# Optimization experiments

Measured on AMD Instinct MI355X. Metric: run time of the kernel, lower is better.

## Reference

```python
import jax, jax.numpy as jnp
import numpy as np

T = 2048          # total tokens
H = 2560          # hidden_size
E = 8             # experts per modality
TOPK = 2          # moe_k
I_TXT = 1536      # moe_intermediate_size[0]
I_IMG = 512       # moe_intermediate_size[1]
I_SH = I_TXT * 2  # shared experts intermediate (moe_num_shared_experts=2)


def setup_inputs() -> dict:
    key = jax.random.key(0)
    ks = jax.random.split(key, 12)
    s = 0.02
    return {
        "hidden_states": jax.random.normal(ks[0], (T, H), jnp.float32),
        "visual_token_mask": jax.random.randint(ks[1], (T, 1), 0, 2).astype(bool),
        # text modality: router gate [E,H], SwiGLU experts [E,H,I]/[E,I,H]
        "text_gate_w": jax.random.normal(ks[2], (E, H), jnp.float32) * s,
        "text_wg": jax.random.normal(ks[3], (E, H, I_TXT), jnp.float32) * s,
        "text_wu": jax.random.normal(ks[4], (E, H, I_TXT), jnp.float32) * s,
        "text_wd": jax.random.normal(ks[5], (E, I_TXT, H), jnp.float32) * s,
        # image modality
        "image_gate_w": jax.random.normal(ks[6], (E, H), jnp.float32) * s,
        "image_wg": jax.random.normal(ks[7], (E, H, I_IMG), jnp.float32) * s,
        "image_wu": jax.random.normal(ks[8], (E, H, I_IMG), jnp.float32) * s,
        "image_wd": jax.random.normal(ks[9], (E, I_IMG, H), jnp.float32) * s,
        # shared experts MLP (dense SwiGLU)
        "sh_wg": jax.random.normal(ks[10], (H, I_SH), jnp.float32) * s,
        "sh_wu": jax.random.normal(ks[11], (H, I_SH), jnp.float32) * s,
        "sh_wd": jax.random.normal(jax.random.fold_in(key, 99), (I_SH, H), jnp.float32) * s,
    }


def _moe(x, gate_w, wg, wu, wd):
    """FusedMoE: softmax router -> top-k -> renormalize -> SwiGLU experts -> combine.
    x: [T,H]; gate_w: [E,H]; wg/wu: [E,H,I]; wd: [E,I,H]."""
    logits = jnp.einsum("th,eh->te", x, gate_w)                 # [T,E]
    probs = jax.nn.softmax(logits.astype(jnp.float32), axis=-1)
    topv, topi = jax.lax.top_k(probs, TOPK)                      # [T,K]
    topv = topv / jnp.sum(topv, axis=-1, keepdims=True)          # renormalize=True
    # dense per-token expert weights [T,E] (zero for unselected experts)
    w = jnp.sum(jax.nn.one_hot(topi, probs.shape[-1], dtype=topv.dtype)
                * topv[..., None], axis=1)
    g = jnp.einsum("th,ehi->tei", x, wg)                         # [T,E,I]
    u = jnp.einsum("th,ehi->tei", x, wu)
    h = jax.nn.silu(g) * u
    y = jnp.einsum("tei,eih->teh", h, wd)                        # [T,E,H]
    return jnp.einsum("te,teh->th", w.astype(x.dtype), y)


def _shared_mlp(x, wg, wu, wd):
    return (jax.nn.silu(x @ wg) * (x @ wu)) @ wd


def reference(hidden_states, visual_token_mask,
              text_gate_w, text_wg, text_wu, text_wd,
              image_gate_w, image_wg, image_wu, image_wd,
              sh_wg, sh_wu, sh_wd):
    x = hidden_states.reshape(-1, hidden_states.shape[-1])       # [T,H]
    shared_out = _shared_mlp(x, sh_wg, sh_wu, sh_wd)
    text_out = _moe(x, text_gate_w, text_wg, text_wu, text_wd)
    image_out = _moe(x, image_gate_w, image_wg, image_wu, image_wd)
    vmask = visual_token_mask.reshape(-1, 1)                     # [T,1] bool
    # scatter-combine: image experts on visual tokens, text experts elsewhere
    final = jnp.where(vmask, image_out, text_out) + shared_out
    return final.reshape(hidden_states.shape)
```

## Files before the change

### kernel.cpp

```cpp
#include <hip/hip_runtime.h>
#include <hip/hip_bf16.h>

#define T 2048
#define H 2560
#define NE 8
#define ITXT 1536
#define IIMG 512
#define ISH 3072
#define CAP 2048

using bf16 = __hip_bfloat16;
typedef short short8 __attribute__((ext_vector_type(8)));
typedef float float4v __attribute__((ext_vector_type(4)));

static constexpr size_t OFF_XBF  = 0;
static constexpr size_t OFF_CNT  = OFF_XBF + (size_t)T * H * 2;
static constexpr size_t OFF_TOK  = OFF_CNT + 128;
static constexpr size_t OFF_WTS  = OFF_TOK + (size_t)17 * CAP * 4;
static constexpr size_t OFF_HTXT = OFF_WTS + (size_t)17 * CAP * 4;
static constexpr size_t OFF_HIMG = OFF_HTXT + (size_t)NE * CAP * ITXT * 2;
static constexpr size_t OFF_HSH  = OFF_HIMG + (size_t)NE * CAP * IIMG * 2;

__device__ __forceinline__ unsigned short f2bf(float f) {
    bf16 b = __float2bfloat16(f);
    unsigned short u;
    __builtin_memcpy(&u, &b, 2);
    return u;
}

__global__ void k_cast_init(const float* __restrict__ x, bf16* __restrict__ xb,
                            int* __restrict__ counts, int* __restrict__ toks,
                            float* __restrict__ wts) {
    int i = blockIdx.x * blockDim.x + threadIdx.x;
    float4 v = ((const float4*)x)[i];
    ushort4 p;
    p.x = f2bf(v.x); p.y = f2bf(v.y); p.z = f2bf(v.z); p.w = f2bf(v.w);
    *(ushort4*)(xb + 4 * (size_t)i) = p;
    if (i < CAP) { toks[16 * CAP + i] = i; wts[16 * CAP + i] = 1.0f; }
    if (i == 0) counts[16] = T;
}

__global__ void k_router(const float* __restrict__ x, const int* __restrict__ vmask,
                         const float* __restrict__ tg, const float* __restrict__ ig,
                         int* __restrict__ counts, int* __restrict__ toks,
                         float* __restrict__ wts) {
    int wave = threadIdx.x >> 6;
    int lane = threadIdx.x & 63;
    int t = blockIdx.x * 4 + wave;
    if (t >= T) return;
    bool vis = vmask[t] != 0;
    const float* gw = vis ? ig : tg;
    const float* xr = x + (size_t)t * H;
    float logits[NE];
#pragma unroll
    for (int e = 0; e < NE; ++e) {
        const float* g = gw + (size_t)e * H;
        double s = 0.0;
        for (int h = lane; h < H; h += 64) s += (double)xr[h] * (double)g[h];
#pragma unroll
        for (int off = 32; off > 0; off >>= 1) s += __shfl_xor(s, off);
        logits[e] = (float)s;
    }
    if (lane == 0) {
        int e1 = 0;
#pragma unroll
        for (int e = 1; e < NE; ++e) if (logits[e] > logits[e1]) e1 = e;
        int e2 = -1;
#pragma unroll
        for (int e = 0; e < NE; ++e)
            if (e != e1 && (e2 < 0 || logits[e] > logits[e2])) e2 = e;
        float w1 = 1.0f / (1.0f + expf(logits[e2] - logits[e1]));
        float w2 = 1.0f - w1;
        int b = vis ? 8 : 0;
        int s1 = atomicAdd(&counts[b + e1], 1);
        toks[(b + e1) * CAP + s1] = t; wts[(b + e1) * CAP + s1] = w1;
        int s2 = atomicAdd(&counts[b + e2], 1);
        toks[(b + e2) * CAP + s2] = t; wts[(b + e2) * CAP + s2] = w2;
    }
}

#define MT 128
#define NT 64
#define BK 32
#define LSTR 40

__global__ __launch_bounds__(256) void k_gateup_all(
    const float* __restrict__ twg, const float* __restrict__ twu,
    const float* __restrict__ iwg, const float* __restrict__ iwu,
    const float* __restrict__ swg, const float* __restrict__ swu,
    const bf16* __restrict__ A,
    const int* __restrict__ counts, const int* __restrict__ toks,
    bf16* __restrict__ htxt, bf16* __restrict__ himg, bf16* __restrict__ hsh) {
    int z = blockIdx.z;
    const float *bg, *bu; int N; bf16* hb;
    if (z < 8) {
        bg = twg + (size_t)z * H * ITXT; bu = twu + (size_t)z * H * ITXT;
        N = ITXT; hb = htxt + (size_t)z * CAP * ITXT;
    } else if (z < 16) {
        int e = z - 8;
        bg = iwg + (size_t)e * H * IIMG; bu = iwu + (size_t)e * H * IIMG;
        N = IIMG; hb = himg + (size_t)e * CAP * IIMG;
    } else {
        bg = swg; bu = swu; N = ISH; hb = hsh;
    }
    int n0 = blockIdx.x * NT;
    if (n0 >= N) return;
    int cnt = counts[z];
    int m0 = blockIdx.y * MT;
    if (m0 >= cnt) return;
    const int* tk = toks + (size_t)z * CAP + m0;

    __shared__ bf16 As[2][MT][LSTR];
    __shared__ bf16 Bs[2][2][NT][LSTR];

    int tid = threadIdx.x;
    int lane = tid & 63;
    int wv = tid >> 6;
    int wm = wv >> 1, wn = wv & 1;

    int ar = tid >> 2;
    int akc = (tid & 3) << 3;
    int bn = (tid & 15) << 2;
    int bk = (tid >> 4) << 1;
    int fr = lane & 15;
    int fk = (lane >> 4) << 3;

    int cl = cnt - m0 - 1;
    int r0 = ar, r1 = ar + 64;
    int t0 = tk[r0 < cl ? r0 : cl];
    int t1 = tk[r1 < cl ? r1 : cl];
    const bf16* aP0 = A + (size_t)t0 * H + akc;
    const bf16* aP1 = A + (size_t)t1 * H + akc;
    const float* pg = bg + (size_t)bk * N + n0 + bn;
    const float* pu = bu + (size_t)bk * N + n0 + bn;

    float4v accg[4][2], accu[4][2];
#pragma unroll
    for (int i = 0; i < 4; ++i)
#pragma unroll
        for (int j = 0; j < 2; ++j) { accg[i][j] = (float4v)0.0f; accu[i][j] = (float4v)0.0f; }

    uint4 a0r, a1r; float4 g0r, g1r, u0r, u1r;
    auto LOADR = [&](int k0) {
        a0r = *(const uint4*)(aP0 + k0);
        a1r = *(const uint4*)(aP1 + k0);
        const float* g = pg + (size_t)k0 * N;
        g0r = *(const float4*)g; g1r = *(const float4*)(g + N);
        const float* u = pu + (size_t)k0 * N;
        u0r = *(const float4*)u; u1r = *(const float4*)(u + N);
    };
    auto STORER = [&](int buf) {
        *(uint4*)&As[buf][ar][akc] = a0r;
        *(uint4*)&As[buf][ar + 64][akc] = a1r;
        *(unsigned*)&Bs[buf][0][bn + 0][bk] = (unsigned)f2bf(g0r.x) | ((unsigned)f2bf(g1r.x) << 16);
        *(unsigned*)&Bs[buf][0][bn + 1][bk] = (unsigned)f2bf(g0r.y) | ((unsigned)f2bf(g1r.y) << 16);
        *(unsigned*)&Bs[buf][0][bn + 2][bk] = (unsigned)f2bf(g0r.z) | ((unsigned)f2bf(g1r.z) << 16);
        *(unsigned*)&Bs[buf][0][bn + 3][bk] = (unsigned)f2bf(g0r.w) | ((unsigned)f2bf(g1r.w) << 16);
        *(unsigned*)&Bs[buf][1][bn + 0][bk] = (unsigned)f2bf(u0r.x) | ((unsigned)f2bf(u1r.x) << 16);
        *(unsigned*)&Bs[buf][1][bn + 1][bk] = (unsigned)f2bf(u0r.y) | ((unsigned)f2bf(u1r.y) << 16);
        *(unsigned*)&Bs[buf][1][bn + 2][bk] = (unsigned)f2bf(u0r.z) | ((unsigned)f2bf(u1r.z) << 16);
        *(unsigned*)&Bs[buf][1][bn + 3][bk] = (unsigned)f2bf(u0r.w) | ((unsigned)f2bf(u1r.w) << 16);
    };

    LOADR(0);
    STORER(0);
    int cur = 0;
    for (int k0 = 0; k0 < H; k0 += BK) {
        __syncthreads();
        bool more = (k0 + BK) < H;
        if (more) LOADR(k0 + BK);
        short8 af[4], bgf[2], buf_[2];
#pragma unroll
        for (int i = 0; i < 4; ++i) af[i] = *(const short8*)&As[cur][wm * 64 + i * 16 + fr][fk];
#pragma unroll
        for (int j = 0; j < 2; ++j) {
            bgf[j]  = *(const short8*)&Bs[cur][0][wn * 32 + j * 16 + fr][fk];
            buf_[j] = *(const short8*)&Bs[cur][1][wn * 32 + j * 16 + fr][fk];
        }
#pragma unroll
        for (int i = 0; i < 4; ++i)
#pragma unroll
            for (int j = 0; j < 2; ++j) {
                accg[i][j] = __builtin_amdgcn_mfma_f32_16x16x32_bf16(af[i], bgf[j],  accg[i][j], 0, 0, 0);
                accu[i][j] = __builtin_amdgcn_mfma_f32_16x16x32_bf16(af[i], buf_[j], accu[i][j], 0, 0, 0);
            }
        if (more) STORER(cur ^ 1);
        cur ^= 1;
    }

    int rbase = (lane >> 4) << 2;
    int cc = lane & 15;
#pragma unroll
    for (int i = 0; i < 4; ++i)
#pragma unroll
        for (int j = 0; j < 2; ++j)
#pragma unroll
            for (int r = 0; r < 4; ++r) {
                int ml = m0 + wm * 64 + i * 16 + rbase + r;
                if (ml < cnt) {
                    int col = n0 + wn * 32 + j * 16 + cc;
                    float g = accg[i][j][r], u = accu[i][j][r];
                    float hv = g / (1.0f + expf(-g)) * u;
                    hb[(size_t)ml * N + col] = __float2bfloat16(hv);
                }
            }
}

__global__ __launch_bounds__(256) void k_down_all(
    const float* __restrict__ twd, const float* __restrict__ iwd, const float* __restrict__ swd,
    const bf16* __restrict__ htxt, const bf16* __restrict__ himg, const bf16* __restrict__ hsh,
    const int* __restrict__ counts, const int* __restrict__ toks,
    const float* __restrict__ wts,
    float* __restrict__ out) {
    int z = blockIdx.z;
    const float* bw; const bf16* Ab; int K;
    if (z < 8) {
        bw = twd + (size_t)z * ITXT * H; Ab = htxt + (size_t)z * CAP * ITXT; K = ITXT;
    } else if (z < 16) {
        int e = z - 8;
        bw = iwd + (size_t)e * IIMG * H; Ab = himg + (size_t)e * CAP * IIMG; K = IIMG;
    } else {
        bw = swd; Ab = hsh; K = ISH;
    }
    int cnt = counts[z];
    int m0 = blockIdx.y * MT;
    if (m0 >= cnt) return;
    int n0 = blockIdx.x * NT;

    __shared__ bf16 As[2][MT][LSTR];
    __shared__ bf16 Bs[2][NT][LSTR];

    int tid = threadIdx.x;
    int lane = tid & 63;
    int wv = tid >> 6;
    int wm = wv >> 1, wn = wv & 1;

    int ar = tid >> 2;
    int akc = (tid & 3) << 3;
    int bn = (tid & 15) << 2;
    int bk = (tid >> 4) << 1;
    int fr = lane & 15;
    int fk = (lane >> 4) << 3;

    const bf16* aP0 = Ab + (size_t)(m0 + ar) * K + akc;
    const bf16* aP1 = Ab + (size_t)(m0 + ar + 64) * K + akc;
    const float* pb = bw + (size_t)bk * H + n0 + bn;

    float4v acc[4][2];
#pragma unroll
    for (int i = 0; i < 4; ++i)
#pragma unroll
        for (int j = 0; j < 2; ++j) acc[i][j] = (float4v)0.0f;

    uint4 a0r, a1r; float4 b0r, b1r;
    auto LOADR = [&](int k0) {
        a0r = *(const uint4*)(aP0 + k0);
        a1r = *(const uint4*)(aP1 + k0);
        const float* s = pb + (size_t)k0 * H;
        b0r = *(const float4*)s; b1r = *(const float4*)(s + H);
    };
    auto STORER = [&](int buf) {
        *(uint4*)&As[buf][ar][akc] = a0r;
        *(uint4*)&As[buf][ar + 64][akc] = a1r;
        *(unsigned*)&Bs[buf][bn + 0][bk] = (unsigned)f2bf(b0r.x) | ((unsigned)f2bf(b1r.x) << 16);
        *(unsigned*)&Bs[buf][bn + 1][bk] = (unsigned)f2bf(b0r.y) | ((unsigned)f2bf(b1r.y) << 16);
        *(unsigned*)&Bs[buf][bn + 2][bk] = (unsigned)f2bf(b0r.z) | ((unsigned)f2bf(b1r.z) << 16);
        *(unsigned*)&Bs[buf][bn + 3][bk] = (unsigned)f2bf(b0r.w) | ((unsigned)f2bf(b1r.w) << 16);
    };

    LOADR(0);
    STORER(0);
    int cur = 0;
    for (int k0 = 0; k0 < K; k0 += BK) {
        __syncthreads();
        bool more = (k0 + BK) < K;
        if (more) LOADR(k0 + BK);
        short8 af[4], bf_[2];
#pragma unroll
        for (int i = 0; i < 4; ++i) af[i] = *(const short8*)&As[cur][wm * 64 + i * 16 + fr][fk];
#pragma unroll
        for (int j = 0; j < 2; ++j) bf_[j] = *(const short8*)&Bs[cur][wn * 32 + j * 16 + fr][fk];
#pragma unroll
        for (int i = 0; i < 4; ++i)
#pragma unroll
            for (int j = 0; j < 2; ++j)
                acc[i][j] = __builtin_amdgcn_mfma_f32_16x16x32_bf16(af[i], bf_[j], acc[i][j], 0, 0, 0);
        if (more) STORER(cur ^ 1);
        cur ^= 1;
    }

    int rbase = (lane >> 4) << 2;
    int cc = lane & 15;
    const int* tkl = toks + (size_t)z * CAP;
    const float* wl = wts + (size_t)z * CAP;
#pragma unroll
    for (int i = 0; i < 4; ++i)
#pragma unroll
        for (int j = 0; j < 2; ++j)
#pragma unroll
            for (int r = 0; r < 4; ++r) {
                int ml = m0 + wm * 64 + i * 16 + rbase + r;
                if (ml < cnt) {
                    int col = n0 + wn * 32 + j * 16 + cc;
                    int tok = tkl[ml];
                    atomicAdd(&out[(size_t)tok * H + col], acc[i][j][r] * wl[ml]);
                }
            }
}

extern "C" void kernel_launch(void* const* d_in, const int* in_sizes, int n_in,
                              void* d_out, int out_size, void* d_ws, size_t ws_size,
                              hipStream_t stream) {
    const float* x    = (const float*)d_in[0];
    const int*   vm   = (const int*)d_in[1];
    const float* tg   = (const float*)d_in[2];
    const float* twg  = (const float*)d_in[3];
    const float* twu  = (const float*)d_in[4];
    const float* twd  = (const float*)d_in[5];
    const float* ig   = (const float*)d_in[6];
    const float* iwg  = (const float*)d_in[7];
    const float* iwu  = (const float*)d_in[8];
    const float* iwd  = (const float*)d_in[9];
    const float* swg  = (const float*)d_in[10];
    const float* swu  = (const float*)d_in[11];
    const float* swd  = (const float*)d_in[12];
    float* out = (float*)d_out;
    char* ws = (char*)d_ws;

    bf16* xb     = (bf16*)(ws + OFF_XBF);
    int*  counts = (int*)(ws + OFF_CNT);
    int*  toks   = (int*)(ws + OFF_TOK);
    float* wtsp  = (float*)(ws + OFF_WTS);
    bf16* htxt   = (bf16*)(ws + OFF_HTXT);
    bf16* himg   = (bf16*)(ws + OFF_HIMG);
    bf16* hsh    = (bf16*)(ws + OFF_HSH);

    hipMemsetAsync(counts, 0, 128, stream);
    hipMemsetAsync(out, 0, (size_t)T * H * sizeof(float), stream);

    k_cast_init<<<dim3((T * H / 4) / 256), dim3(256), 0, stream>>>(x, xb, counts, toks, wtsp);
    k_router<<<dim3(T / 4), dim3(256), 0, stream>>>(x, vm, tg, ig, counts, toks, wtsp);

    k_gateup_all<<<dim3(ISH / NT, CAP / MT, 17), dim3(256), 0, stream>>>(
        twg, twu, iwg, iwu, swg, swu, xb, counts, toks, htxt, himg, hsh);

    k_down_all<<<dim3(H / NT, CAP / MT, 17), dim3(256), 0, stream>>>(
        twd, iwd, swd, htxt, himg, hsh, counts, toks, wtsp, out);
}
```

Measured before the change: 1.134 ms.

## Pre-transpose weights to bf16 K-major with swizzled LDS and BK=64

Adds a per-call transpose kernel that converts every fp32 weight matrix into bf16 laid out N-major with K contiguous. The GEMMs then load weights with 16-byte vector loads and skip the in-loop fp32-to-bf16 conversion, which was scattered across many narrow LDS stores. LDS tiles become unpadded with an XOR swizzle, and the K step doubles to 64. The shared-expert down projection now writes its output directly instead of using atomics, which removes the output memset. In exchange, every call re-reads all fp32 weights and writes a bf16 copy in extra launches.

```diff
diff --git a/kernel.cpp b/kernel.cpp
--- a/kernel.cpp
+++ b/kernel.cpp
@@ -20,12 +20,46 @@
 static constexpr size_t OFF_HTXT = OFF_WTS + (size_t)17 * CAP * 4;
 static constexpr size_t OFF_HIMG = OFF_HTXT + (size_t)NE * CAP * ITXT * 2;
 static constexpr size_t OFF_HSH  = OFF_HIMG + (size_t)NE * CAP * IIMG * 2;
+static constexpr size_t OFF_TGT  = OFF_HSH + (size_t)CAP * ISH * 2;
+static constexpr size_t OFF_TUT  = OFF_TGT + (size_t)NE * ITXT * H * 2;
+static constexpr size_t OFF_TDT  = OFF_TUT + (size_t)NE * ITXT * H * 2;
+static constexpr size_t OFF_IGT  = OFF_TDT + (size_t)NE * H * ITXT * 2;
+static constexpr size_t OFF_IUT  = OFF_IGT + (size_t)NE * IIMG * H * 2;
+static constexpr size_t OFF_IDT  = OFF_IUT + (size_t)NE * IIMG * H * 2;
+static constexpr size_t OFF_SGT  = OFF_IDT + (size_t)NE * H * IIMG * 2;
+static constexpr size_t OFF_SUT  = OFF_SGT + (size_t)ISH * H * 2;
+static constexpr size_t OFF_SDT  = OFF_SUT + (size_t)ISH * H * 2;
 
 __device__ __forceinline__ unsigned short f2bf(float f) {
     bf16 b = __float2bfloat16(f);
     unsigned short u;
     __builtin_memcpy(&u, &b, 2);
     return u;
+}
+
+__global__ __launch_bounds__(256) void k_w2t(const float* __restrict__ in,
+                                             bf16* __restrict__ out, int K, int N) {
+    size_t zo = (size_t)K * N * blockIdx.z;
+    in += zo; out += zo;
+    __shared__ float s[64][65];
+    int t = threadIdx.x;
+    int k0 = blockIdx.y * 64, n0 = blockIdx.x * 64;
+    int tr = t >> 4, tc = (t & 15) * 4;
+#pragma unroll
+    for (int p = 0; p < 4; ++p) {
+        float4 v = *(const float4*)(in + (size_t)(k0 + p * 16 + tr) * N + n0 + tc);
+        int r = p * 16 + tr;
+        s[r][tc] = v.x; s[r][tc + 1] = v.y; s[r][tc + 2] = v.z; s[r][tc + 3] = v.w;
+    }
+    __syncthreads();
+#pragma unroll
+    for (int p = 0; p < 4; ++p) {
+        int n = p * 16 + tr;
+        ushort4 o;
+        o.x = f2bf(s[tc + 0][n]); o.y = f2bf(s[tc + 1][n]);
+        o.z = f2bf(s[tc + 2][n]); o.w = f2bf(s[tc + 3][n]);
+        *(ushort4*)(out + (size_t)(n0 + n) * K + k0 + tc) = o;
+    }
 }
 
 __global__ void k_cast_init(const float* __restrict__ x, bf16* __restrict__ xb,
@@ -81,27 +115,26 @@
 
 #define MT 128
 #define NT 64
-#define BK 32
-#define LSTR 40
+#define BKG 64
 
 __global__ __launch_bounds__(256) void k_gateup_all(
-    const float* __restrict__ twg, const float* __restrict__ twu,
-    const float* __restrict__ iwg, const float* __restrict__ iwu,
-    const float* __restrict__ swg, const float* __restrict__ swu,
+    const bf16* __restrict__ tgT, const bf16* __restrict__ tuT,
+    const bf16* __restrict__ igT, const bf16* __restrict__ iuT,
+    const bf16* __restrict__ sgT, const bf16* __restrict__ suT,
     const bf16* __restrict__ A,
     const int* __restrict__ counts, const int* __restrict__ toks,
     bf16* __restrict__ htxt, bf16* __restrict__ himg, bf16* __restrict__ hsh) {
     int z = blockIdx.z;
-    const float *bg, *bu; int N; bf16* hb;
+    const bf16 *bg, *bu; int N; bf16* hb;
     if (z < 8) {
-        bg = twg + (size_t)z * H * ITXT; bu = twu + (size_t)z * H * ITXT;
+        bg = tgT + (size_t)z * ITXT * H; bu = tuT + (size_t)z * ITXT * H;
         N = ITXT; hb = htxt + (size_t)z * CAP * ITXT;
     } else if (z < 16) {
         int e = z - 8;
-        bg = iwg + (size_t)e * H * IIMG; bu = iwu + (size_t)e * H * IIMG;
+        bg = igT + (size_t)e * IIMG * H; bu = iuT + (size_t)e * IIMG * H;
         N = IIMG; hb = himg + (size_t)e * CAP * IIMG;
     } else {
-        bg = swg; bu = swu; N = ISH; hb = hsh;
+        bg = sgT; bu = suT; N = ISH; hb = hsh;
     }
     int n0 = blockIdx.x * NT;
     if (n0 >= N) return;
@@ -110,29 +143,40 @@
     if (m0 >= cnt) return;
     const int* tk = toks + (size_t)z * CAP + m0;
 
-    __shared__ bf16 As[2][MT][LSTR];
-    __shared__ bf16 Bs[2][2][NT][LSTR];
-
-    int tid = threadIdx.x;
-    int lane = tid & 63;
-    int wv = tid >> 6;
+    __shared__ bf16 As[2][MT * BKG];
+    __shared__ bf16 Bs[2][2][NT * BKG];
+
+    int t = threadIdx.x, lane = t & 63, wv = t >> 6;
     int wm = wv >> 1, wn = wv & 1;
 
-    int ar = tid >> 2;
-    int akc = (tid & 3) << 3;
-    int bn = (tid & 15) << 2;
-    int bk = (tid >> 4) << 1;
-    int fr = lane & 15;
-    int fk = (lane >> 4) << 3;
-
+    int sA = t & 7, rA = t >> 3, vA = rA & 7;
     int cl = cnt - m0 - 1;
-    int r0 = ar, r1 = ar + 64;
-    int t0 = tk[r0 < cl ? r0 : cl];
-    int t1 = tk[r1 < cl ? r1 : cl];
-    const bf16* aP0 = A + (size_t)t0 * H + akc;
-    const bf16* aP1 = A + (size_t)t1 * H + akc;
-    const float* pg = bg + (size_t)bk * N + n0 + bn;
-    const float* pu = bu + (size_t)bk * N + n0 + bn;
+    const bf16* aP[4]; int dA[4];
+#pragma unroll
+    for (int h = 0; h < 4; ++h) {
+        int r = rA + h * 32;
+        int rr = r < cl ? r : cl;
+        aP[h] = A + (size_t)tk[rr] * H + sA * 8;
+        dA[h] = r * BKG + ((sA ^ vA) << 3);
+    }
+    int nB = t >> 2, sB = (t & 3) * 2, vB = nB & 7;
+    const bf16* gP = bg + (size_t)(n0 + nB) * H + sB * 8;
+    const bf16* uP = bu + (size_t)(n0 + nB) * H + sB * 8;
+    int dB0 = nB * BKG + (((sB) ^ vB) << 3);
+    int dB1 = nB * BKG + (((sB + 1) ^ vB) << 3);
+
+    int fr = lane & 15, hi = lane >> 4, vF = fr & 7;
+    int oA[4][2], oB[2][2];
+#pragma unroll
+    for (int i = 0; i < 4; ++i)
+#pragma unroll
+        for (int s = 0; s < 2; ++s)
+            oA[i][s] = (wm * 64 + i * 16 + fr) * BKG + (((s * 4 + hi) ^ vF) << 3);
+#pragma unroll
+    for (int j = 0; j < 2; ++j)
+#pragma unroll
+        for (int s = 0; s < 2; ++s)
+            oB[j][s] = (wn * 32 + j * 16 + fr) * BKG + (((s * 4 + hi) ^ vF) << 3);
 
     float4v accg[4][2], accu[4][2];
 #pragma unroll
@@ -140,56 +184,51 @@
 #pragma unroll
         for (int j = 0; j < 2; ++j) { accg[i][j] = (float4v)0.0f; accu[i][j] = (float4v)0.0f; }
 
-    uint4 a0r, a1r; float4 g0r, g1r, u0r, u1r;
+    uint4 a_[4], g_[2], u_[2];
     auto LOADR = [&](int k0) {
-        a0r = *(const uint4*)(aP0 + k0);
-        a1r = *(const uint4*)(aP1 + k0);
-        const float* g = pg + (size_t)k0 * N;
-        g0r = *(const float4*)g; g1r = *(const float4*)(g + N);
-        const float* u = pu + (size_t)k0 * N;
-        u0r = *(const float4*)u; u1r = *(const float4*)(u + N);
+#pragma unroll
+        for (int h = 0; h < 4; ++h) a_[h] = *(const uint4*)(aP[h] + k0);
+        g_[0] = *(const uint4*)(gP + k0); g_[1] = *(const uint4*)(gP + k0 + 8);
+        u_[0] = *(const uint4*)(uP + k0); u_[1] = *(const uint4*)(uP + k0 + 8);
     };
     auto STORER = [&](int buf) {
-        *(uint4*)&As[buf][ar][akc] = a0r;
-        *(uint4*)&As[buf][ar + 64][akc] = a1r;
-        *(unsigned*)&Bs[buf][0][bn + 0][bk] = (unsigned)f2bf(g0r.x) | ((unsigned)f2bf(g1r.x) << 16);
-        *(unsigned*)&Bs[buf][0][bn + 1][bk] = (unsigned)f2bf(g0r.y) | ((unsigned)f2bf(g1r.y) << 16);
-        *(unsigned*)&Bs[buf][0][bn + 2][bk] = (unsigned)f2bf(g0r.z) | ((unsigned)f2bf(g1r.z) << 16);
-        *(unsigned*)&Bs[buf][0][bn + 3][bk] = (unsigned)f2bf(g0r.w) | ((unsigned)f2bf(g1r.w) << 16);
-        *(unsigned*)&Bs[buf][1][bn + 0][bk] = (unsigned)f2bf(u0r.x) | ((unsigned)f2bf(u1r.x) << 16);
-        *(unsigned*)&Bs[buf][1][bn + 1][bk] = (unsigned)f2bf(u0r.y) | ((unsigned)f2bf(u1r.y) << 16);
-        *(unsigned*)&Bs[buf][1][bn + 2][bk] = (unsigned)f2bf(u0r.z) | ((unsigned)f2bf(u1r.z) << 16);
-        *(unsigned*)&Bs[buf][1][bn + 3][bk] = (unsigned)f2bf(u0r.w) | ((unsigned)f2bf(u1r.w) << 16);
+#pragma unroll
+        for (int h = 0; h < 4; ++h) *(uint4*)&As[buf][dA[h]] = a_[h];
+        *(uint4*)&Bs[buf][0][dB0] = g_[0]; *(uint4*)&Bs[buf][0][dB1] = g_[1];
+        *(uint4*)&Bs[buf][1][dB0] = u_[0]; *(uint4*)&Bs[buf][1][dB1] = u_[1];
     };
 
     LOADR(0);
     STORER(0);
     int cur = 0;
-    for (int k0 = 0; k0 < H; k0 += BK) {
+    for (int k0 = 0; k0 < H; k0 += BKG) {
         __syncthreads();
-        bool more = (k0 + BK) < H;
-        if (more) LOADR(k0 + BK);
-        short8 af[4], bgf[2], buf_[2];
-#pragma unroll
-        for (int i = 0; i < 4; ++i) af[i] = *(const short8*)&As[cur][wm * 64 + i * 16 + fr][fk];
-#pragma unroll
-        for (int j = 0; j < 2; ++j) {
-            bgf[j]  = *(const short8*)&Bs[cur][0][wn * 32 + j * 16 + fr][fk];
-            buf_[j] = *(const short8*)&Bs[cur][1][wn * 32 + j * 16 + fr][fk];
+        bool more = (k0 + BKG) < H;
+        if (more) LOADR(k0 + BKG);
+#pragma unroll
+        for (int s = 0; s < 2; ++s) {
+            short8 af[4], bgf[2], buf_[2];
+#pragma unroll
+            for (int i = 0; i < 4; ++i) af[i] = *(const short8*)&As[cur][oA[i][s]];
+#pragma unroll
+            for (int j = 0; j < 2; ++j) {
+                bgf[j]  = *(const short8*)&Bs[cur][0][oB[j][s]];
+                buf_[j] = *(const short8*)&Bs[cur][1][oB[j][s]];
+            }
+#pragma unroll
+            for (int i = 0; i < 4; ++i)
+#pragma unroll
+                for (int j = 0; j < 2; ++j) {
+                    accg[i][j] = __builtin_amdgcn_mfma_f32_16x16x32_bf16(af[i], bgf[j],  accg[i][j], 0, 0, 0);
+                    accu[i][j] = __builtin_amdgcn_mfma_f32_16x16x32_bf16(af[i], buf_[j], accu[i][j], 0, 0, 0);
+                }
         }
-#pragma unroll
-        for (int i = 0; i < 4; ++i)
-#pragma unroll
-            for (int j = 0; j < 2; ++j) {
-                accg[i][j] = __builtin_amdgcn_mfma_f32_16x16x32_bf16(af[i], bgf[j],  accg[i][j], 0, 0, 0);
-                accu[i][j] = __builtin_amdgcn_mfma_f32_16x16x32_bf16(af[i], buf_[j], accu[i][j], 0, 0, 0);
-            }
         if (more) STORER(cur ^ 1);
         cur ^= 1;
     }
 
-    int rbase = (lane >> 4) << 2;
-    int cc = lane & 15;
+    int rbase = hi << 2;
+    int cc = fr;
 #pragma unroll
     for (int i = 0; i < 4; ++i)
 #pragma unroll
@@ -206,45 +245,53 @@
             }
 }
 
-__global__ __launch_bounds__(256) void k_down_all(
-    const float* __restrict__ twd, const float* __restrict__ iwd, const float* __restrict__ swd,
+template <bool SH>
+__global__ __launch_bounds__(256) void k_down(
+    const bf16* __restrict__ tdT, const bf16* __restrict__ idT, const bf16* __restrict__ sdT,
     const bf16* __restrict__ htxt, const bf16* __restrict__ himg, const bf16* __restrict__ hsh,
     const int* __restrict__ counts, const int* __restrict__ toks,
     const float* __restrict__ wts,
     float* __restrict__ out) {
-    int z = blockIdx.z;
-    const float* bw; const bf16* Ab; int K;
-    if (z < 8) {
-        bw = twd + (size_t)z * ITXT * H; Ab = htxt + (size_t)z * CAP * ITXT; K = ITXT;
-    } else if (z < 16) {
-        int e = z - 8;
-        bw = iwd + (size_t)e * IIMG * H; Ab = himg + (size_t)e * CAP * IIMG; K = IIMG;
-    } else {
-        bw = swd; Ab = hsh; K = ISH;
-    }
-    int cnt = counts[z];
+    int z = SH ? 16 : blockIdx.z;
+    const bf16 *bw, *Ab; int K, cnt;
+    if (SH) { bw = sdT; Ab = hsh; K = ISH; cnt = T; }
+    else if (z < 8) { bw = tdT + (size_t)z * H * ITXT; Ab = htxt + (size_t)z * CAP * ITXT; K = ITXT; cnt = counts[z]; }
+    else { int e = z - 8; bw = idT + (size_t)e * H * IIMG; Ab = himg + (size_t)e * CAP * IIMG; K = IIMG; cnt = counts[z]; }
     int m0 = blockIdx.y * MT;
     if (m0 >= cnt) return;
     int n0 = blockIdx.x * NT;
 
-    __shared__ bf16 As[2][MT][LSTR];
-    __shared__ bf16 Bs[2][NT][LSTR];
-
-    int tid = threadIdx.x;
-    int lane = tid & 63;
-    int wv = tid >> 6;
+    __shared__ bf16 As[2][MT * BKG];
+    __shared__ bf16 Bs[2][NT * BKG];
+
+    int t = threadIdx.x, lane = t & 63, wv = t >> 6;
     int wm = wv >> 1, wn = wv & 1;
 
-    int ar = tid >> 2;
-    int akc = (tid & 3) << 3;
-    int bn = (tid & 15) << 2;
-    int bk = (tid >> 4) << 1;
-    int fr = lane & 15;
-    int fk = (lane >> 4) << 3;
-
-    const bf16* aP0 = Ab + (size_t)(m0 + ar) * K + akc;
-    const bf16* aP1 = Ab + (size_t)(m0 + ar + 64) * K + akc;
-    const float* pb = bw + (size_t)bk * H + n0 + bn;
+    int sA = t & 7, rA = t >> 3, vA = rA & 7;
+    const bf16* aP[4]; int dA[4];
+#pragma unroll
+    for (int h = 0; h < 4; ++h) {
+        int r = rA + h * 32;
+        aP[h] = Ab + (size_t)(m0 + r) * K + sA * 8;
+        dA[h] = r * BKG + ((sA ^ vA) << 3);
+    }
+    int nB = t >> 2, sB = (t & 3) * 2, vB = nB & 7;
+    const bf16* bP = bw + (size_t)(n0 + nB) * K + sB * 8;
+    int dB0 = nB * BKG + (((sB) ^ vB) << 3);
+    int dB1 = nB * BKG + (((sB + 1) ^ vB) << 3);
+
+    int fr = lane & 15, hi = lane >> 4, vF = fr & 7;
+    int oA[4][2], oB[2][2];
+#pragma unroll
+    for (int i = 0; i < 4; ++i)
+#pragma unroll
+        for (int s = 0; s < 2; ++s)
+            oA[i][s] = (wm * 64 + i * 16 + fr) * BKG + (((s * 4 + hi) ^ vF) << 3);
+#pragma unroll
+    for (int j = 0; j < 2; ++j)
+#pragma unroll
+        for (int s = 0; s < 2; ++s)
+            oB[j][s] = (wn * 32 + j * 16 + fr) * BKG + (((s * 4 + hi) ^ vF) << 3);
 
     float4v acc[4][2];
 #pragma unroll
@@ -252,45 +299,44 @@
 #pragma unroll
         for (int j = 0; j < 2; ++j) acc[i][j] = (float4v)0.0f;
 
-    uint4 a0r, a1r; float4 b0r, b1r;
+    uint4 a_[4], b_[2];
     auto LOADR = [&](int k0) {
-        a0r = *(const uint4*)(aP0 + k0);
-        a1r = *(const uint4*)(aP1 + k0);
-        const float* s = pb + (size_t)k0 * H;
-        b0r = *(const float4*)s; b1r = *(const float4*)(s + H);
+#pragma unroll
+        for (int h = 0; h < 4; ++h) a_[h] = *(const uint4*)(aP[h] + k0);
+        b_[0] = *(const uint4*)(bP + k0); b_[1] = *(const uint4*)(bP + k0 + 8);
     };
     auto STORER = [&](int buf) {
-        *(uint4*)&As[buf][ar][akc] = a0r;
-        *(uint4*)&As[buf][ar + 64][akc] = a1r;
-        *(unsigned*)&Bs[buf][bn + 0][bk] = (unsigned)f2bf(b0r.x) | ((unsigned)f2bf(b1r.x) << 16);
-        *(unsigned*)&Bs[buf][bn + 1][bk] = (unsigned)f2bf(b0r.y) | ((unsigned)f2bf(b1r.y) << 16);
-        *(unsigned*)&Bs[buf][bn + 2][bk] = (unsigned)f2bf(b0r.z) | ((unsigned)f2bf(b1r.z) << 16);
-        *(unsigned*)&Bs[buf][bn + 3][bk] = (unsigned)f2bf(b0r.w) | ((unsigned)f2bf(b1r.w) << 16);
+#pragma unroll
+        for (int h = 0; h < 4; ++h) *(uint4*)&As[buf][dA[h]] = a_[h];
+        *(uint4*)&Bs[buf][dB0] = b_[0]; *(uint4*)&Bs[buf][dB1] = b_[1];
     };
 
     LOADR(0);
     STORER(0);
     int cur = 0;
-    for (int k0 = 0; k0 < K; k0 += BK) {
+    for (int k0 = 0; k0 < K; k0 += BKG) {
         __syncthreads();
-        bool more = (k0 + BK) < K;
-        if (more) LOADR(k0 + BK);
-        short8 af[4], bf_[2];
-#pragma unroll
-        for (int i = 0; i < 4; ++i) af[i] = *(const short8*)&As[cur][wm * 64 + i * 16 + fr][fk];
-#pragma unroll
-        for (int j = 0; j < 2; ++j) bf_[j] = *(const short8*)&Bs[cur][wn * 32 + j * 16 + fr][fk];
-#pragma unroll
-        for (int i = 0; i < 4; ++i)
-#pragma unroll
-            for (int j = 0; j < 2; ++j)
-                acc[i][j] = __builtin_amdgcn_mfma_f32_16x16x32_bf16(af[i], bf_[j], acc[i][j], 0, 0, 0);
+        bool more = (k0 + BKG) < K;
+        if (more) LOADR(k0 + BKG);
+#pragma unroll
+        for (int s = 0; s < 2; ++s) {
+            short8 af[4], bf_[2];
+#pragma unroll
+            for (int i = 0; i < 4; ++i) af[i] = *(const short8*)&As[cur][oA[i][s]];
+#pragma unroll
+            for (int j = 0; j < 2; ++j) bf_[j] = *(const short8*)&Bs[cur][oB[j][s]];
+#pragma unroll
+            for (int i = 0; i < 4; ++i)
+#pragma unroll
+                for (int j = 0; j < 2; ++j)
+                    acc[i][j] = __builtin_amdgcn_mfma_f32_16x16x32_bf16(af[i], bf_[j], acc[i][j], 0, 0, 0);
+        }
         if (more) STORER(cur ^ 1);
         cur ^= 1;
     }
 
-    int rbase = (lane >> 4) << 2;
-    int cc = lane & 15;
+    int rbase = hi << 2;
+    int cc = fr;
     const int* tkl = toks + (size_t)z * CAP;
     const float* wl = wts + (size_t)z * CAP;
 #pragma unroll
@@ -302,8 +348,11 @@
                 int ml = m0 + wm * 64 + i * 16 + rbase + r;
                 if (ml < cnt) {
                     int col = n0 + wn * 32 + j * 16 + cc;
-                    int tok = tkl[ml];
-                    atomicAdd(&out[(size_t)tok * H + col], acc[i][j][r] * wl[ml]);
+                    if (SH) {
+                        out[(size_t)ml * H + col] = acc[i][j][r];
+                    } else {
+                        atomicAdd(&out[(size_t)tkl[ml] * H + col], acc[i][j][r] * wl[ml]);
+                    }
                 }
             }
 }
@@ -334,16 +383,36 @@
     bf16* htxt   = (bf16*)(ws + OFF_HTXT);
     bf16* himg   = (bf16*)(ws + OFF_HIMG);
     bf16* hsh    = (bf16*)(ws + OFF_HSH);
+    bf16* tgT    = (bf16*)(ws + OFF_TGT);
+    bf16* tuT    = (bf16*)(ws + OFF_TUT);
+    bf16* tdT    = (bf16*)(ws + OFF_TDT);
+    bf16* igT    = (bf16*)(ws + OFF_IGT);
+    bf16* iuT    = (bf16*)(ws + OFF_IUT);
+    bf16* idT    = (bf16*)(ws + OFF_IDT);
+    bf16* sgT    = (bf16*)(ws + OFF_SGT);
+    bf16* suT    = (bf16*)(ws + OFF_SUT);
+    bf16* sdT    = (bf16*)(ws + OFF_SDT);
 
     hipMemsetAsync(counts, 0, 128, stream);
-    hipMemsetAsync(out, 0, (size_t)T * H * sizeof(float), stream);
+
+    k_w2t<<<dim3(ITXT / 64, H / 64, NE), dim3(256), 0, stream>>>(twg, tgT, H, ITXT);
+    k_w2t<<<dim3(ITXT / 64, H / 64, NE), dim3(256), 0, stream>>>(twu, tuT, H, ITXT);
+    k_w2t<<<dim3(H / 64, ITXT / 64, NE), dim3(256), 0, stream>>>(twd, tdT, ITXT, H);
+    k_w2t<<<dim3(IIMG / 64, H / 64, NE), dim3(256), 0, stream>>>(iwg, igT, H, IIMG);
+    k_w2t<<<dim3(IIMG / 64, H / 64, NE), dim3(256), 0, stream>>>(iwu, iuT, H, IIMG);
+    k_w2t<<<dim3(H / 64, IIMG / 64, NE), dim3(256), 0, stream>>>(iwd, idT, IIMG, H);
+    k_w2t<<<dim3(ISH / 64, H / 64, 1), dim3(256), 0, stream>>>(swg, sgT, H, ISH);
+    k_w2t<<<dim3(ISH / 64, H / 64, 1), dim3(256), 0, stream>>>(swu, suT, H, ISH);
+    k_w2t<<<dim3(H / 64, ISH / 64, 1), dim3(256), 0, stream>>>(swd, sdT, ISH, H);
 
     k_cast_init<<<dim3((T * H / 4) / 256), dim3(256), 0, stream>>>(x, xb, counts, toks, wtsp);
     k_router<<<dim3(T / 4), dim3(256), 0, stream>>>(x, vm, tg, ig, counts, toks, wtsp);
 
     k_gateup_all<<<dim3(ISH / NT, CAP / MT, 17), dim3(256), 0, stream>>>(
-        twg, twu, iwg, iwu, swg, swu, xb, counts, toks, htxt, himg, hsh);
-
-    k_down_all<<<dim3(H / NT, CAP / MT, 17), dim3(256), 0, stream>>>(
-        twd, iwd, swd, htxt, himg, hsh, counts, toks, wtsp, out);
-}
+        tgT, tuT, igT, iuT, sgT, suT, xb, counts, toks, htxt, himg, hsh);
+
+    k_down<true><<<dim3(H / NT, CAP / MT, 1), dim3(256), 0, stream>>>(
+        tdT, idT, sdT, htxt, himg, hsh, counts, toks, wtsp, out);
+    k_down<false><<<dim3(H / NT, CAP / MT, 16), dim3(256), 0, stream>>>(
+        tdT, idT, sdT, htxt, himg, hsh, counts, toks, wtsp, out);
+}
```

Measured after the change: 1.645 ms. 1.45x slower.

## Swizzle LDS tiles, vectorize B stores, and prefetch two stages ahead

Applied to the files above, without the earlier changes.

Replaces the padded LDS tile layout with an unpadded layout that uses an XOR swizzle to avoid bank conflicts. Each thread now loads a column of 16 (or 8) fp32 weights along K and writes them to LDS as one or two 128-bit stores, replacing many 32-bit scattered stores. Global loads move to after the LDS store of the previous stage, so the load for the tile after next is in flight during the next MMA step. The cost is that B global loads become scalar strided loads (coalesced across lanes rather than float4 per lane), with a different register footprint.

```diff
diff --git a/kernel.cpp b/kernel.cpp
--- a/kernel.cpp
+++ b/kernel.cpp
@@ -26,6 +26,9 @@
     unsigned short u;
     __builtin_memcpy(&u, &b, 2);
     return u;
+}
+__device__ __forceinline__ unsigned pk2(float a, float b) {
+    return (unsigned)f2bf(a) | ((unsigned)f2bf(b) << 16);
 }
 
 __global__ void k_cast_init(const float* __restrict__ x, bf16* __restrict__ xb,
@@ -82,7 +85,6 @@
 #define MT 128
 #define NT 64
 #define BK 32
-#define LSTR 40
 
 __global__ __launch_bounds__(256) void k_gateup_all(
     const float* __restrict__ twg, const float* __restrict__ twu,
@@ -110,29 +112,35 @@
     if (m0 >= cnt) return;
     const int* tk = toks + (size_t)z * CAP + m0;
 
-    __shared__ bf16 As[2][MT][LSTR];
-    __shared__ bf16 Bs[2][2][NT][LSTR];
-
-    int tid = threadIdx.x;
-    int lane = tid & 63;
-    int wv = tid >> 6;
+    __shared__ bf16 As[2][MT * BK];
+    __shared__ bf16 Bs[2][2][NT * BK];
+
+    int t = threadIdx.x, lane = t & 63, wv = t >> 6;
     int wm = wv >> 1, wn = wv & 1;
 
-    int ar = tid >> 2;
-    int akc = (tid & 3) << 3;
-    int bn = (tid & 15) << 2;
-    int bk = (tid >> 4) << 1;
-    int fr = lane & 15;
-    int fk = (lane >> 4) << 3;
-
+    int rA = t >> 1, hA = t & 1;
     int cl = cnt - m0 - 1;
-    int r0 = ar, r1 = ar + 64;
-    int t0 = tk[r0 < cl ? r0 : cl];
-    int t1 = tk[r1 < cl ? r1 : cl];
-    const bf16* aP0 = A + (size_t)t0 * H + akc;
-    const bf16* aP1 = A + (size_t)t1 * H + akc;
-    const float* pg = bg + (size_t)bk * N + n0 + bn;
-    const float* pu = bu + (size_t)bk * N + n0 + bn;
+    int rr = rA < cl ? rA : cl;
+    const bf16* aP = A + (size_t)tk[rr] * H + hA * 16;
+    int swA = (rA >> 1) & 3;
+    int dA0 = rA * BK + ((2 * hA) ^ swA) * 8;
+    int dA1 = rA * BK + ((2 * hA + 1) ^ swA) * 8;
+
+    int nB = t & 63, sel = t >> 6;
+    int mat = sel >> 1, kh = sel & 1;
+    const float* bBase = (mat ? bu : bg) + (size_t)(kh * 16) * N + n0 + nB;
+    int swB = (nB >> 1) & 3;
+    int dB0 = nB * BK + ((2 * kh) ^ swB) * 8;
+    int dB1 = nB * BK + ((2 * kh + 1) ^ swB) * 8;
+
+    int fr = lane & 15, hi = lane >> 4;
+    int swF = (fr >> 1) & 3;
+    int fo = (hi ^ swF) * 8;
+    int oA[4], oB[2];
+#pragma unroll
+    for (int i = 0; i < 4; ++i) oA[i] = (wm * 64 + i * 16 + fr) * BK + fo;
+#pragma unroll
+    for (int j = 0; j < 2; ++j) oB[j] = (wn * 32 + j * 16 + fr) * BK + fo;
 
     float4v accg[4][2], accu[4][2];
 #pragma unroll
@@ -140,42 +148,40 @@
 #pragma unroll
         for (int j = 0; j < 2; ++j) { accg[i][j] = (float4v)0.0f; accu[i][j] = (float4v)0.0f; }
 
-    uint4 a0r, a1r; float4 g0r, g1r, u0r, u1r;
+    uint4 a0, a1;
+    float bv[16];
     auto LOADR = [&](int k0) {
-        a0r = *(const uint4*)(aP0 + k0);
-        a1r = *(const uint4*)(aP1 + k0);
-        const float* g = pg + (size_t)k0 * N;
-        g0r = *(const float4*)g; g1r = *(const float4*)(g + N);
-        const float* u = pu + (size_t)k0 * N;
-        u0r = *(const float4*)u; u1r = *(const float4*)(u + N);
+        a0 = *(const uint4*)(aP + k0);
+        a1 = *(const uint4*)(aP + k0 + 8);
+        const float* p = bBase + (size_t)k0 * N;
+#pragma unroll
+        for (int i = 0; i < 16; ++i) { bv[i] = *p; p += N; }
     };
     auto STORER = [&](int buf) {
-        *(uint4*)&As[buf][ar][akc] = a0r;
-        *(uint4*)&As[buf][ar + 64][akc] = a1r;
-        *(unsigned*)&Bs[buf][0][bn + 0][bk] = (unsigned)f2bf(g0r.x) | ((unsigned)f2bf(g1r.x) << 16);
-        *(unsigned*)&Bs[buf][0][bn + 1][bk] = (unsigned)f2bf(g0r.y) | ((unsigned)f2bf(g1r.y) << 16);
-        *(unsigned*)&Bs[buf][0][bn + 2][bk] = (unsigned)f2bf(g0r.z) | ((unsigned)f2bf(g1r.z) << 16);
-        *(unsigned*)&Bs[buf][0][bn + 3][bk] = (unsigned)f2bf(g0r.w) | ((unsigned)f2bf(g1r.w) << 16);
-        *(unsigned*)&Bs[buf][1][bn + 0][bk] = (unsigned)f2bf(u0r.x) | ((unsigned)f2bf(u1r.x) << 16);
-        *(unsigned*)&Bs[buf][1][bn + 1][bk] = (unsigned)f2bf(u0r.y) | ((unsigned)f2bf(u1r.y) << 16);
-        *(unsigned*)&Bs[buf][1][bn + 2][bk] = (unsigned)f2bf(u0r.z) | ((unsigned)f2bf(u1r.z) << 16);
-        *(unsigned*)&Bs[buf][1][bn + 3][bk] = (unsigned)f2bf(u0r.w) | ((unsigned)f2bf(u1r.w) << 16);
+        *(uint4*)&As[buf][dA0] = a0;
+        *(uint4*)&As[buf][dA1] = a1;
+        uint4 q0, q1;
+        q0.x = pk2(bv[0], bv[1]);  q0.y = pk2(bv[2], bv[3]);
+        q0.z = pk2(bv[4], bv[5]);  q0.w = pk2(bv[6], bv[7]);
+        q1.x = pk2(bv[8], bv[9]);  q1.y = pk2(bv[10], bv[11]);
+        q1.z = pk2(bv[12], bv[13]); q1.w = pk2(bv[14], bv[15]);
+        *(uint4*)&Bs[buf][mat][dB0] = q0;
+        *(uint4*)&Bs[buf][mat][dB1] = q1;
     };
 
     LOADR(0);
     STORER(0);
+    LOADR(BK);
     int cur = 0;
     for (int k0 = 0; k0 < H; k0 += BK) {
         __syncthreads();
-        bool more = (k0 + BK) < H;
-        if (more) LOADR(k0 + BK);
         short8 af[4], bgf[2], buf_[2];
 #pragma unroll
-        for (int i = 0; i < 4; ++i) af[i] = *(const short8*)&As[cur][wm * 64 + i * 16 + fr][fk];
+        for (int i = 0; i < 4; ++i) af[i] = *(const short8*)&As[cur][oA[i]];
 #pragma unroll
         for (int j = 0; j < 2; ++j) {
-            bgf[j]  = *(const short8*)&Bs[cur][0][wn * 32 + j * 16 + fr][fk];
-            buf_[j] = *(const short8*)&Bs[cur][1][wn * 32 + j * 16 + fr][fk];
+            bgf[j]  = *(const short8*)&Bs[cur][0][oB[j]];
+            buf_[j] = *(const short8*)&Bs[cur][1][oB[j]];
         }
 #pragma unroll
         for (int i = 0; i < 4; ++i)
@@ -184,12 +190,15 @@
                 accg[i][j] = __builtin_amdgcn_mfma_f32_16x16x32_bf16(af[i], bgf[j],  accg[i][j], 0, 0, 0);
                 accu[i][j] = __builtin_amdgcn_mfma_f32_16x16x32_bf16(af[i], buf_[j], accu[i][j], 0, 0, 0);
             }
-        if (more) STORER(cur ^ 1);
-        cur ^= 1;
-    }
-
-    int rbase = (lane >> 4) << 2;
-    int cc = lane & 15;
+        if (k0 + BK < H) {
+            STORER(cur ^ 1);
+            if (k0 + 2 * BK < H) LOADR(k0 + 2 * BK);
+            cur ^= 1;
+        }
+    }
+
+    int rbase = hi << 2;
+    int cc = fr;
 #pragma unroll
     for (int i = 0; i < 4; ++i)
 #pragma unroll
@@ -213,38 +222,39 @@
     const float* __restrict__ wts,
     float* __restrict__ out) {
     int z = blockIdx.z;
-    const float* bw; const bf16* Ab; int K;
-    if (z < 8) {
-        bw = twd + (size_t)z * ITXT * H; Ab = htxt + (size_t)z * CAP * ITXT; K = ITXT;
-    } else if (z < 16) {
-        int e = z - 8;
-        bw = iwd + (size_t)e * IIMG * H; Ab = himg + (size_t)e * CAP * IIMG; K = IIMG;
-    } else {
-        bw = swd; Ab = hsh; K = ISH;
-    }
-    int cnt = counts[z];
+    const float* bw; const bf16* Ab; int K, cnt;
+    if (z < 8) { bw = twd + (size_t)z * ITXT * H; Ab = htxt + (size_t)z * CAP * ITXT; K = ITXT; cnt = counts[z]; }
+    else if (z < 16) { int e = z - 8; bw = iwd + (size_t)e * IIMG * H; Ab = himg + (size_t)e * CAP * IIMG; K = IIMG; cnt = counts[z]; }
+    else { bw = swd; Ab = hsh; K = ISH; cnt = T; }
     int m0 = blockIdx.y * MT;
     if (m0 >= cnt) return;
     int n0 = blockIdx.x * NT;
 
-    __shared__ bf16 As[2][MT][LSTR];
-    __shared__ bf16 Bs[2][NT][LSTR];
-
-    int tid = threadIdx.x;
-    int lane = tid & 63;
-    int wv = tid >> 6;
+    __shared__ bf16 As[2][MT * BK];
+    __shared__ bf16 Bs[2][NT * BK];
+
+    int t = threadIdx.x, lane = t & 63, wv = t >> 6;
     int wm = wv >> 1, wn = wv & 1;
 
-    int ar = tid >> 2;
-    int akc = (tid & 3) << 3;
-    int bn = (tid & 15) << 2;
-    int bk = (tid >> 4) << 1;
-    int fr = lane & 15;
-    int fk = (lane >> 4) << 3;
-
-    const bf16* aP0 = Ab + (size_t)(m0 + ar) * K + akc;
-    const bf16* aP1 = Ab + (size_t)(m0 + ar + 64) * K + akc;
-    const float* pb = bw + (size_t)bk * H + n0 + bn;
+    int rA = t >> 1, hA = t & 1;
+    const bf16* aP = Ab + (size_t)(m0 + rA) * K + hA * 16;
+    int swA = (rA >> 1) & 3;
+    int dA0 = rA * BK + ((2 * hA) ^ swA) * 8;
+    int dA1 = rA * BK + ((2 * hA + 1) ^ swA) * 8;
+
+    int nB = t & 63, kq = t >> 6;
+    const float* bBase = bw + (size_t)(kq * 8) * H + n0 + nB;
+    int swB = (nB >> 1) & 3;
+    int dB0 = nB * BK + (kq ^ swB) * 8;
+
+    int fr = lane & 15, hi = lane >> 4;
+    int swF = (fr >> 1) & 3;
+    int fo = (hi ^ swF) * 8;
+    int oA[4], oB[2];
+#pragma unroll
+    for (int i = 0; i < 4; ++i) oA[i] = (wm * 64 + i * 16 + fr) * BK + fo;
+#pragma unroll
+    for (int j = 0; j < 2; ++j) oB[j] = (wn * 32 + j * 16 + fr) * BK + fo;
 
     float4v acc[4][2];
 #pragma unroll
@@ -252,45 +262,49 @@
 #pragma unroll
         for (int j = 0; j < 2; ++j) acc[i][j] = (float4v)0.0f;
 
-    uint4 a0r, a1r; float4 b0r, b1r;
+    uint4 a0, a1;
+    float bv[8];
     auto LOADR = [&](int k0) {
-        a0r = *(const uint4*)(aP0 + k0);
-        a1r = *(const uint4*)(aP1 + k0);
-        const float* s = pb + (size_t)k0 * H;
-        b0r = *(const float4*)s; b1r = *(const float4*)(s + H);
+        a0 = *(const uint4*)(aP + k0);
+        a1 = *(const uint4*)(aP + k0 + 8);
+        const float* p = bBase + (size_t)k0 * H;
+#pragma unroll
+        for (int i = 0; i < 8; ++i) { bv[i] = *p; p += H; }
     };
     auto STORER = [&](int buf) {
-        *(uint4*)&As[buf][ar][akc] = a0r;
-        *(uint4*)&As[buf][ar + 64][akc] = a1r;
-        *(unsigned*)&Bs[buf][bn + 0][bk] = (unsigned)f2bf(b0r.x) | ((unsigned)f2bf(b1r.x) << 16);
-        *(unsigned*)&Bs[buf][bn + 1][bk] = (unsigned)f2bf(b0r.y) | ((unsigned)f2bf(b1r.y) << 16);
-        *(unsigned*)&Bs[buf][bn + 2][bk] = (unsigned)f2bf(b0r.z) | ((unsigned)f2bf(b1r.z) << 16);
-        *(unsigned*)&Bs[buf][bn + 3][bk] = (unsigned)f2bf(b0r.w) | ((unsigned)f2bf(b1r.w) << 16);
+        *(uint4*)&As[buf][dA0] = a0;
+        *(uint4*)&As[buf][dA1] = a1;
+        uint4 q0;
+        q0.x = pk2(bv[0], bv[1]); q0.y = pk2(bv[2], bv[3]);
+        q0.z = pk2(bv[4], bv[5]); q0.w = pk2(bv[6], bv[7]);
+        *(uint4*)&Bs[buf][dB0] = q0;
     };
 
     LOADR(0);
     STORER(0);
+    LOADR(BK);
     int cur = 0;
     for (int k0 = 0; k0 < K; k0 += BK) {
         __syncthreads();
-        bool more = (k0 + BK) < K;
-        if (more) LOADR(k0 + BK);
         short8 af[4], bf_[2];
 #pragma unroll
-        for (int i = 0; i < 4; ++i) af[i] = *(const short8*)&As[cur][wm * 64 + i * 16 + fr][fk];
-#pragma unroll
-        for (int j = 0; j < 2; ++j) bf_[j] = *(const short8*)&Bs[cur][wn * 32 + j * 16 + fr][fk];
+        for (int i = 0; i < 4; ++i) af[i] = *(const short8*)&As[cur][oA[i]];
+#pragma unroll
+        for (int j = 0; j < 2; ++j) bf_[j] = *(const short8*)&Bs[cur][oB[j]];
 #pragma unroll
         for (int i = 0; i < 4; ++i)
 #pragma unroll
             for (int j = 0; j < 2; ++j)
                 acc[i][j] = __builtin_amdgcn_mfma_f32_16x16x32_bf16(af[i], bf_[j], acc[i][j], 0, 0, 0);
-        if (more) STORER(cur ^ 1);
-        cur ^= 1;
-    }
-
-    int rbase = (lane >> 4) << 2;
-    int cc = lane & 15;
+        if (k0 + BK < K) {
+            STORER(cur ^ 1);
+            if (k0 + 2 * BK < K) LOADR(k0 + 2 * BK);
+            cur ^= 1;
+        }
+    }
+
+    int rbase = hi << 2;
+    int cc = fr;
     const int* tkl = toks + (size_t)z * CAP;
     const float* wl = wts + (size_t)z * CAP;
 #pragma unroll
```

New measurement: 1.074 ms. 5.3% less time.
